# Performance work log

Hardware: AMD Instinct MI355X
Metric: run time of the kernel (lower is better)

The kernel has to match this reference:

```python
import jax, jax.numpy as jnp
import numpy as np

TOKENS = 1024
IN_W = 512
BLOCK = 256
OUT_W = 512
N_BLOCKS = 64
K = 2


def setup_inputs() -> dict:
    key = jax.random.key(0)
    ks = jax.random.split(key, 8)
    u = lambda k, s: jax.random.uniform(k, s, jnp.float32, -1.0, 1.0)
    return {
        "x": jax.random.normal(ks[0], (TOKENS, IN_W), jnp.float32),
        "noise": jax.random.normal(ks[1], (TOKENS, N_BLOCKS), jnp.float32),
        "w1s": u(ks[2], (N_BLOCKS, IN_W, BLOCK)),
        "b1s": u(ks[3], (N_BLOCKS, BLOCK)),
        "w2s": u(ks[4], (N_BLOCKS, BLOCK, OUT_W)),
        "b2s": u(ks[5], (N_BLOCKS, OUT_W)),
        "mixer": jnp.zeros((IN_W, N_BLOCKS), jnp.float32) + 0.01 * jax.random.normal(ks[6], (IN_W, N_BLOCKS), jnp.float32),
        "noise_controller": jnp.zeros((IN_W, N_BLOCKS), jnp.float32) + 0.01 * jax.random.normal(ks[7], (IN_W, N_BLOCKS), jnp.float32),
        "k": K,
    }


def reference(x, noise, w1s, b1s, w2s, b2s, mixer, noise_controller, k):
    # noisy routing logits: mixer_prod + randn * softplus(noise_prod)
    h_x = x @ mixer + noise * jax.nn.softplus(x @ noise_controller)  # [B, E]
    topk_vals, topk_idx = jax.lax.top_k(h_x, k)                       # [B, K]
    scores = jax.nn.softmax(topk_vals, axis=-1)                       # [B, K]
    # per-token expert weight gather (faithful to index_select semantics)
    gw1 = w1s[topk_idx]  # [B, K, I, H]
    gb1 = b1s[topk_idx]  # [B, K, H]
    gw2 = w2s[topk_idx]  # [B, K, H, O]
    gb2 = b2s[topk_idx]  # [B, K, O]
    v = jax.nn.relu(jnp.einsum('bi,bkih->bkh', x, gw1) + gb1)        # [B, K, H]
    out = jnp.einsum('bkh,bkho->bko', v, gw2) + gb2                   # [B, K, O]
    return jnp.sum(out * scores[..., None], axis=1)                   # [B, O]
```

## Files before the change

### kernel.cpp

```cpp
#include <hip/hip_runtime.h>
#include <math.h>

#define TOKENS    1024
#define IN_W      512
#define BLOCK_H   256
#define OUT_W     512
#define N_EXPERTS 64
#define TOPK      2
#define NSLOTS    (TOKENS * TOPK)
#define LIST_CAP  128
#define T_CAP     12
#define NGRP      4
#define XPAD      520
#define VPAD      264

__device__ __forceinline__ void red_xor(float4& v, int m) {
    v.x += __shfl_xor(v.x, m); v.y += __shfl_xor(v.y, m);
    v.z += __shfl_xor(v.z, m); v.w += __shfl_xor(v.w, m);
}

__device__ __forceinline__ void fma4(float4& a, float s, const float4& w) {
    a.x = fmaf(s, w.x, a.x); a.y = fmaf(s, w.y, a.y);
    a.z = fmaf(s, w.z, a.z); a.w = fmaf(s, w.w, a.w);
}

__global__ __launch_bounds__(256) void routing_kernel(
    const float* __restrict__ x, const float* __restrict__ noise,
    const float* __restrict__ mixer, const float* __restrict__ noisec,
    float* __restrict__ esc, int* __restrict__ counts, int* __restrict__ lists,
    float* __restrict__ out)
{
    __shared__ float xs[512];
    __shared__ float pm[4 * 64];
    __shared__ float pn[4 * 64];
    __shared__ float hs[64];
    const int t    = blockIdx.x;
    const int tid  = threadIdx.x;
    const int wave = tid >> 6, lane = tid & 63;
    const int rs   = lane >> 4;
    const int c    = lane & 15;

    if (tid < 128) {
        ((float4*)xs)[tid] = ((const float4*)(x + (size_t)t * IN_W))[tid];
        ((float4*)(out + (size_t)t * OUT_W))[tid] = make_float4(0.f, 0.f, 0.f, 0.f);
    }
    __syncthreads();

    float4 am = make_float4(0.f, 0.f, 0.f, 0.f), an = am;
    const float4* m4 = (const float4*)mixer;
    const float4* n4 = (const float4*)noisec;
    const int rbase = wave * 128;
    #pragma unroll 4
    for (int j = 0; j < 32; ++j) {
        const int r = rbase + j * 4 + rs;
        const float xv = xs[r];
        const float4 wm = m4[r * 16 + c];
        const float4 wn = n4[r * 16 + c];
        fma4(am, xv, wm);
        fma4(an, xv, wn);
    }
    red_xor(am, 16); red_xor(am, 32);
    red_xor(an, 16); red_xor(an, 32);
    if (lane < 16) {
        *(float4*)&pm[wave * 64 + lane * 4] = am;
        *(float4*)&pn[wave * 64 + lane * 4] = an;
    }
    __syncthreads();

    if (tid < 64) {
        const float am2 = pm[tid] + pm[64 + tid] + pm[128 + tid] + pm[192 + tid];
        const float an2 = pn[tid] + pn[64 + tid] + pn[128 + tid] + pn[192 + tid];
        const float sp = fmaxf(an2, 0.f) + log1pf(expf(-fabsf(an2)));
        hs[tid] = am2 + noise[(size_t)t * 64 + tid] * sp;
    }
    __syncthreads();

    if (tid == 0) {
        float b0 = -INFINITY, b1 = -INFINITY;
        int i0 = 0, i1 = 0;
        for (int i = 0; i < N_EXPERTS; ++i) {
            const float v = hs[i];
            if (v > b0)      { b1 = b0; i1 = i0; b0 = v; i0 = i; }
            else if (v > b1) { b1 = v; i1 = i; }
        }
        const float z   = expf(b1 - b0);
        const float inv = 1.f / (1.f + z);
        esc[t * 2 + 0] = inv;
        esc[t * 2 + 1] = z * inv;
        const int p0 = atomicAdd(&counts[i0], 1);
        if (p0 < LIST_CAP) lists[i0 * LIST_CAP + p0] = t * 2 + 0;
        const int p1 = atomicAdd(&counts[i1], 1);
        if (p1 < LIST_CAP) lists[i1 * LIST_CAP + p1] = t * 2 + 1;
    }
}

template<int T>
__device__ __forceinline__ void run_pass(
    int nTok, int wave, int lane,
    const float4* __restrict__ w1v, const float4* __restrict__ w2v,
    const float4* __restrict__ b1v, const float4* __restrict__ b2v,
    const float* __restrict__ xs, float* __restrict__ vsm,
    const int* __restrict__ slotIds, const float* __restrict__ escv,
    float* __restrict__ out)
{
    {
        const int c4l = lane & 3, r0 = lane >> 2;
        float4 acc[T];
        #pragma unroll
        for (int t = 0; t < T; ++t) acc[t] = make_float4(0.f, 0.f, 0.f, 0.f);
        const float4* wp = w1v + (size_t)(r0 * 64 + wave * 4 + c4l);
        const float*  xb = xs + r0;
        #pragma unroll 2
        for (int s = 0; s < 32; ++s) {
            const float4 w = wp[(size_t)s * 1024];
            #pragma unroll
            for (int t = 0; t < T; ++t) {
                const float xv = xb[t * XPAD + s * 16];
                acc[t].x = fmaf(xv, w.x, acc[t].x);
                acc[t].y = fmaf(xv, w.y, acc[t].y);
                acc[t].z = fmaf(xv, w.z, acc[t].z);
                acc[t].w = fmaf(xv, w.w, acc[t].w);
            }
        }
        #pragma unroll
        for (int t = 0; t < T; ++t) {
            red_xor(acc[t], 4); red_xor(acc[t], 8);
            red_xor(acc[t], 16); red_xor(acc[t], 32);
        }
        if (r0 == 0) {
            const float4 bb = b1v[wave * 4 + c4l];
            #pragma unroll
            for (int t = 0; t < T; ++t) {
                float4 r;
                r.x = fmaxf(acc[t].x + bb.x, 0.f);
                r.y = fmaxf(acc[t].y + bb.y, 0.f);
                r.z = fmaxf(acc[t].z + bb.z, 0.f);
                r.w = fmaxf(acc[t].w + bb.w, 0.f);
                *(float4*)&vsm[t * VPAD + wave * 16 + c4l * 4] = r;
            }
        }
    }
    __syncthreads();

    {
        const int c8 = lane & 7, r8 = lane >> 3;
        float4 acc[T];
        #pragma unroll
        for (int t = 0; t < T; ++t) acc[t] = make_float4(0.f, 0.f, 0.f, 0.f);
        const float4* wp = w2v + (size_t)(r8 * 128 + wave * 8 + c8);
        const float*  vb = vsm + r8;
        #pragma unroll 2
        for (int s = 0; s < 32; ++s) {
            const float4 w = wp[(size_t)s * 1024];
            #pragma unroll
            for (int t = 0; t < T; ++t) {
                const float vv = vb[t * VPAD + s * 8];
                acc[t].x = fmaf(vv, w.x, acc[t].x);
                acc[t].y = fmaf(vv, w.y, acc[t].y);
                acc[t].z = fmaf(vv, w.z, acc[t].z);
                acc[t].w = fmaf(vv, w.w, acc[t].w);
            }
        }
        #pragma unroll
        for (int t = 0; t < T; ++t) {
            red_xor(acc[t], 8); red_xor(acc[t], 16); red_xor(acc[t], 32);
        }
        const float4 bb = b2v[wave * 8 + c8];
        #pragma unroll
        for (int t = 0; t < T; ++t) {
            if ((t & 7) == r8 && t < nTok) {
                const float sc = escv[t];
                float* o = out + (size_t)(slotIds[t] >> 1) * OUT_W
                               + (wave * 8 + c8) * 4;
                atomicAdd(o + 0, (acc[t].x + bb.x) * sc);
                atomicAdd(o + 1, (acc[t].y + bb.y) * sc);
                atomicAdd(o + 2, (acc[t].z + bb.z) * sc);
                atomicAdd(o + 3, (acc[t].w + bb.w) * sc);
            }
        }
    }
}

__global__ __launch_bounds__(1024, 4) void expert_kernel(
    const float* __restrict__ x,
    const float* __restrict__ w1s, const float* __restrict__ b1s,
    const float* __restrict__ w2s, const float* __restrict__ b2s,
    const int* __restrict__ counts, const int* __restrict__ lists,
    const float* __restrict__ esc, float* __restrict__ out)
{
    __shared__ __align__(16) float xs[T_CAP * XPAD];
    __shared__ __align__(16) float vsm[T_CAP * VPAD];
    __shared__ int   slotIds[T_CAP];
    __shared__ float escv[T_CAP];

    const int e  = blockIdx.x;
    const int g  = blockIdx.y;
    const int ne = min(counts[e], LIST_CAP);
    const int tid  = threadIdx.x;
    const int wave = tid >> 6, lane = tid & 63;

    const float4* w1v = (const float4*)(w1s + (size_t)e * IN_W * BLOCK_H);
    const float4* w2v = (const float4*)(w2s + (size_t)e * BLOCK_H * OUT_W);
    const float4* b1v = (const float4*)(b1s + (size_t)e * BLOCK_H);
    const float4* b2v = (const float4*)(b2s + (size_t)e * OUT_W);
    const float4* x4  = (const float4*)x;

    for (int s0 = g; s0 < ne; s0 += NGRP * T_CAP) {
        const int nTok  = min(T_CAP, (ne - s0 + NGRP - 1) / NGRP);
        const int Tpath = (nTok <= 4) ? 4 : (nTok <= 8) ? 8 : 12;

        if (tid < T_CAP) {
            int s = 0; float sc = 0.f;
            if (tid < nTok) { s = lists[e * LIST_CAP + s0 + tid * NGRP]; sc = esc[s]; }
            slotIds[tid] = s;
            escv[tid]    = sc;
        }
        __syncthreads();

        for (int idx = tid; idx < Tpath * 128; idx += 1024) {
            const int t = idx >> 7, q = idx & 127;
            float4 v = make_float4(0.f, 0.f, 0.f, 0.f);
            if (t < nTok) v = x4[(size_t)(slotIds[t] >> 1) * 128 + q];
            *(float4*)&xs[t * XPAD + q * 4] = v;
        }
        __syncthreads();

        if (nTok <= 4)
            run_pass<4>(nTok, wave, lane, w1v, w2v, b1v, b2v, xs, vsm, slotIds, escv, out);
        else if (nTok <= 8)
            run_pass<8>(nTok, wave, lane, w1v, w2v, b1v, b2v, xs, vsm, slotIds, escv, out);
        else
            run_pass<12>(nTok, wave, lane, w1v, w2v, b1v, b2v, xs, vsm, slotIds, escv, out);
        __syncthreads();
    }
}

extern "C" void kernel_launch(void* const* d_in, const int* in_sizes, int n_in,
                              void* d_out, int out_size, void* d_ws, size_t ws_size,
                              hipStream_t stream) {
    const float* x      = (const float*)d_in[0];
    const float* noise  = (const float*)d_in[1];
    const float* w1s    = (const float*)d_in[2];
    const float* b1s    = (const float*)d_in[3];
    const float* w2s    = (const float*)d_in[4];
    const float* b2s    = (const float*)d_in[5];
    const float* mixer  = (const float*)d_in[6];
    const float* noisec = (const float*)d_in[7];
    float* out = (float*)d_out;

    char* ws = (char*)d_ws;
    int*   counts = (int*)ws;                       ws += 256;
    float* esc    = (float*)ws;                     ws += NSLOTS * sizeof(float);
    int*   lists  = (int*)ws;

    hipMemsetAsync(counts, 0, 256, stream);

    routing_kernel<<<TOKENS, 256, 0, stream>>>(x, noise, mixer, noisec,
                                               esc, counts, lists, out);
    expert_kernel<<<dim3(N_EXPERTS, NGRP), 1024, 0, stream>>>(
        x, w1s, b1s, w2s, b2s, counts, lists, esc, out);
}
```

Baseline: 168.8 us.

## Double-buffer expert weight chunks into LDS via async global_load_lds

Both expert matmul phases now stream their weights through a double-buffered 64 KB LDS region, filled with asynchronous global-to-LDS loads (`__builtin_amdgcn_global_load_lds`). The next chunk is prefetched while the current one is consumed, and the first W2 chunk is prefetched during the last W1 iteration. The aim is to hide global memory latency behind the FMA work. In exchange it adds a block-wide barrier per chunk and much more LDS per block, which likely limits residency to one 1024-thread block per CU. Each weight element is still read by only one lane, so the LDS hop adds no data reuse.

```diff
diff --git a/kernel.cpp b/kernel.cpp
--- a/kernel.cpp
+++ b/kernel.cpp
@@ -94,12 +94,41 @@
     }
 }
 
+
+__device__ __forceinline__ void stage_w1_chunk(const char* w1e, int k, float* dst,
+                                               int wave, int lane) {
+    #pragma unroll
+    for (int j = 0; j < 2; ++j) {
+        const int row = k * 32 + j * 16 + (lane >> 2);
+        const int c4  = wave * 4 + (lane & 3);
+        const char* g = w1e + (size_t)row * 1024 + c4 * 16;
+        float* l = dst + (j * 16 + wave) * 256;
+        __builtin_amdgcn_global_load_lds(
+            (const __attribute__((address_space(1))) void*)g,
+            (__attribute__((address_space(3))) void*)l, 16, 0, 0);
+    }
+}
+
+__device__ __forceinline__ void stage_w2_chunk(const char* w2e, int k, float* dst,
+                                               int wave, int lane) {
+    #pragma unroll
+    for (int j = 0; j < 2; ++j) {
+        const int row = k * 16 + j * 8 + (lane >> 3);
+        const int c4  = wave * 8 + (lane & 7);
+        const char* g = w2e + (size_t)row * 2048 + c4 * 16;
+        float* l = dst + (j * 16 + wave) * 256;
+        __builtin_amdgcn_global_load_lds(
+            (const __attribute__((address_space(1))) void*)g,
+            (__attribute__((address_space(3))) void*)l, 16, 0, 0);
+    }
+}
+
 template<int T>
 __device__ __forceinline__ void run_pass(
     int nTok, int wave, int lane,
-    const float4* __restrict__ w1v, const float4* __restrict__ w2v,
+    const char* w1e, const char* w2e,
     const float4* __restrict__ b1v, const float4* __restrict__ b2v,
-    const float* __restrict__ xs, float* __restrict__ vsm,
+    const float* __restrict__ xs, float* __restrict__ vsm, float* __restrict__ wlds,
     const int* __restrict__ slotIds, const float* __restrict__ escv,
     float* __restrict__ out)
 {
@@ -108,19 +137,22 @@
         float4 acc[T];
         #pragma unroll
         for (int t = 0; t < T; ++t) acc[t] = make_float4(0.f, 0.f, 0.f, 0.f);
-        const float4* wp = w1v + (size_t)(r0 * 64 + wave * 4 + c4l);
-        const float*  xb = xs + r0;
-        #pragma unroll 2
-        for (int s = 0; s < 32; ++s) {
-            const float4 w = wp[(size_t)s * 1024];
+        const float* xb = xs + r0;
+        for (int k = 0; k < 16; ++k) {
+            if (k + 1 < 16) stage_w1_chunk(w1e, k + 1, wlds + ((k + 1) & 1) * 8192, wave, lane);
+            else            stage_w2_chunk(w2e, 0,     wlds + 0 * 8192, wave, lane);
+            const float* cb = wlds + (k & 1) * 8192;
             #pragma unroll
-            for (int t = 0; t < T; ++t) {
-                const float xv = xb[t * XPAD + s * 16];
-                acc[t].x = fmaf(xv, w.x, acc[t].x);
-                acc[t].y = fmaf(xv, w.y, acc[t].y);
-                acc[t].z = fmaf(xv, w.z, acc[t].z);
-                acc[t].w = fmaf(xv, w.w, acc[t].w);
-            }
+            for (int j = 0; j < 2; ++j) {
+                const float4 w = *(const float4*)&cb[(j * 16 + wave) * 256 + lane * 4];
+                const int s = k * 2 + j;
+                #pragma unroll
+                for (int t = 0; t < T; ++t) {
+                    const float xv = xb[t * XPAD + s * 16];
+                    fma4(acc[t], xv, w);
+                }
+            }
+            __syncthreads();
         }
         #pragma unroll
         for (int t = 0; t < T; ++t) {
@@ -147,19 +179,21 @@
         float4 acc[T];
         #pragma unroll
         for (int t = 0; t < T; ++t) acc[t] = make_float4(0.f, 0.f, 0.f, 0.f);
-        const float4* wp = w2v + (size_t)(r8 * 128 + wave * 8 + c8);
-        const float*  vb = vsm + r8;
-        #pragma unroll 2
-        for (int s = 0; s < 32; ++s) {
-            const float4 w = wp[(size_t)s * 1024];
+        const float* vb = vsm + r8;
+        for (int k = 0; k < 16; ++k) {
+            if (k + 1 < 16) stage_w2_chunk(w2e, k + 1, wlds + ((k + 1) & 1) * 8192, wave, lane);
+            const float* cb = wlds + (k & 1) * 8192;
             #pragma unroll
-            for (int t = 0; t < T; ++t) {
-                const float vv = vb[t * VPAD + s * 8];
-                acc[t].x = fmaf(vv, w.x, acc[t].x);
-                acc[t].y = fmaf(vv, w.y, acc[t].y);
-                acc[t].z = fmaf(vv, w.z, acc[t].z);
-                acc[t].w = fmaf(vv, w.w, acc[t].w);
-            }
+            for (int j = 0; j < 2; ++j) {
+                const float4 w = *(const float4*)&cb[(j * 16 + wave) * 256 + lane * 4];
+                const int s = k * 2 + j;
+                #pragma unroll
+                for (int t = 0; t < T; ++t) {
+                    const float vv = vb[t * VPAD + s * 8];
+                    fma4(acc[t], vv, w);
+                }
+            }
+            __syncthreads();
         }
         #pragma unroll
         for (int t = 0; t < T; ++t) {
@@ -188,6 +222,7 @@
     const int* __restrict__ counts, const int* __restrict__ lists,
     const float* __restrict__ esc, float* __restrict__ out)
 {
+    __shared__ __align__(16) float wlds[2 * 8192];
     __shared__ __align__(16) float xs[T_CAP * XPAD];
     __shared__ __align__(16) float vsm[T_CAP * VPAD];
     __shared__ int   slotIds[T_CAP];
@@ -199,8 +234,8 @@
     const int tid  = threadIdx.x;
     const int wave = tid >> 6, lane = tid & 63;
 
-    const float4* w1v = (const float4*)(w1s + (size_t)e * IN_W * BLOCK_H);
-    const float4* w2v = (const float4*)(w2s + (size_t)e * BLOCK_H * OUT_W);
+    const char* w1e = (const char*)(w1s + (size_t)e * IN_W * BLOCK_H);
+    const char* w2e = (const char*)(w2s + (size_t)e * BLOCK_H * OUT_W);
     const float4* b1v = (const float4*)(b1s + (size_t)e * BLOCK_H);
     const float4* b2v = (const float4*)(b2s + (size_t)e * OUT_W);
     const float4* x4  = (const float4*)x;
@@ -217,6 +252,7 @@
         }
         __syncthreads();
 
+        stage_w1_chunk(w1e, 0, wlds, wave, lane);
         for (int idx = tid; idx < Tpath * 128; idx += 1024) {
             const int t = idx >> 7, q = idx & 127;
             float4 v = make_float4(0.f, 0.f, 0.f, 0.f);
@@ -226,11 +262,11 @@
         __syncthreads();
 
         if (nTok <= 4)
-            run_pass<4>(nTok, wave, lane, w1v, w2v, b1v, b2v, xs, vsm, slotIds, escv, out);
+            run_pass<4>(nTok, wave, lane, w1e, w2e, b1v, b2v, xs, vsm, wlds, slotIds, escv, out);
         else if (nTok <= 8)
-            run_pass<8>(nTok, wave, lane, w1v, w2v, b1v, b2v, xs, vsm, slotIds, escv, out);
+            run_pass<8>(nTok, wave, lane, w1e, w2e, b1v, b2v, xs, vsm, wlds, slotIds, escv, out);
         else
-            run_pass<12>(nTok, wave, lane, w1v, w2v, b1v, b2v, xs, vsm, slotIds, escv, out);
+            run_pass<12>(nTok, wave, lane, w1e, w2e, b1v, b2v, xs, vsm, wlds, slotIds, escv, out);
         __syncthreads();
     }
 }
```

Result: slower. 226.8 us (+34.4%).
